# Optimization experiments

Hardware: AMD Instinct MI355X
Metric: run time of the kernel (lower is better)

Reference implementation:

```python
import jax, jax.numpy as jnp
import numpy as np

NUM_HEADS = 16
HEAD_DIM = 64
TOP_K_TILES = 8
TILE_SIZE = 16
ROPE_BASE = 10000.0


def make_freqs_cis(seq_len, head_dim):
    # [seq, head_dim//2] complex64, standard RoPE frequencies
    inv_freq = 1.0 / (ROPE_BASE ** (jnp.arange(0, head_dim, 2, dtype=jnp.float32) / head_dim))
    angles = jnp.arange(seq_len, dtype=jnp.float32)[:, None] * inv_freq[None, :]
    return jax.lax.complex(jnp.cos(angles), jnp.sin(angles))


def apply_rope(xq, xk, freqs_cis):
    # xq, xk: [b, h, s, d]; pairs adjacent channels as (real, imag)
    xq_ = xq.astype(jnp.float32).reshape(*xq.shape[:-1], -1, 2)
    xk_ = xk.astype(jnp.float32).reshape(*xk.shape[:-1], -1, 2)
    xq_c = jax.lax.complex(xq_[..., 0], xq_[..., 1])
    xk_c = jax.lax.complex(xk_[..., 0], xk_[..., 1])
    f = freqs_cis[None, None, :xq.shape[2], :]
    xq_r = xq_c * f
    xk_r = xk_c * f
    xq_out = jnp.stack([xq_r.real, xq_r.imag], axis=-1).reshape(xq.shape)
    xk_out = jnp.stack([xk_r.real, xk_r.imag], axis=-1).reshape(xk.shape)
    return xq_out.astype(xq.dtype), xk_out.astype(xk.dtype)


def setup_inputs() -> dict:
    key = jax.random.key(0)
    ks = jax.random.split(key, 5)
    B, S, D = 2, 2048, 1024
    scale = 1.0 / np.sqrt(D)
    return {
        "x": jax.random.normal(ks[0], (B, S, D), dtype=jnp.float32),
        "wq": jax.random.normal(ks[1], (D, NUM_HEADS * HEAD_DIM), dtype=jnp.float32) * scale,
        "wk": jax.random.normal(ks[2], (D, NUM_HEADS * HEAD_DIM), dtype=jnp.float32) * scale,
        "wv": jax.random.normal(ks[3], (D, NUM_HEADS * HEAD_DIM), dtype=jnp.float32) * scale,
        "wo": jax.random.normal(ks[4], (NUM_HEADS * HEAD_DIM, D), dtype=jnp.float32) * scale,
    }


def reference(x, wq, wk, wv, wo):
    batch, seq_len, _ = x.shape
    q = (x @ wq).reshape(batch, seq_len, NUM_HEADS, HEAD_DIM)
    k = (x @ wk).reshape(batch, seq_len, NUM_HEADS, HEAD_DIM)
    v = (x @ wv).reshape(batch, seq_len, NUM_HEADS, HEAD_DIM)

    freqs_cis = make_freqs_cis(seq_len, HEAD_DIM)
    q_t = jnp.transpose(q, (0, 2, 1, 3))
    k_t = jnp.transpose(k, (0, 2, 1, 3))
    q_t, k_t = apply_rope(q_t, k_t, freqs_cis)
    q = jnp.transpose(q_t, (0, 2, 1, 3))
    k = jnp.transpose(k_t, (0, 2, 1, 3))

    logits = jnp.einsum('bqhd,bkhd->bhqk', q, k) / jnp.sqrt(jnp.float32(HEAD_DIM))
    causal = jnp.tril(jnp.ones((seq_len, seq_len), dtype=bool))
    logits = jnp.where(causal[None, None, :, :], logits, -1e10)
    weights = jax.nn.softmax(logits, axis=-1)  # [b, h, q, k]

    # Scout: tile-max-pool last token's attention probs + top-k tile selection
    last_token_probs = weights[:, :, -1, :]  # [b, h, k]
    pad_len = (TILE_SIZE - seq_len % TILE_SIZE) % TILE_SIZE
    if pad_len > 0:
        last_token_probs = jnp.pad(last_token_probs, ((0, 0), (0, 0), (0, pad_len)))
    num_tiles = last_token_probs.shape[-1] // TILE_SIZE
    tile_scores = jnp.max(
        last_token_probs.reshape(batch, NUM_HEADS, num_tiles, TILE_SIZE), axis=-1)
    _, top_tile_indices = jax.lax.top_k(tile_scores, TOP_K_TILES)  # [b, h, top_k]

    output = jnp.einsum('bhqk,bkhd->bqhd', weights, v)
    output = output.reshape(batch, seq_len, NUM_HEADS * HEAD_DIM)
    output = output @ wo
    return output, top_tile_indices
```

## Files before the change

kernel.cpp:

```cpp
#include <hip/hip_runtime.h>

#define B_ 2
#define S_ 2048
#define E_ 1024
#define H_ 16
#define D_ 64
#define BS_ (B_*S_)
#define PSTR 76

typedef unsigned short u16;
typedef __attribute__((ext_vector_type(8))) short short8;
typedef __attribute__((ext_vector_type(4))) float floatx4;
typedef __bf16 bf16x8 __attribute__((ext_vector_type(8)));

__device__ __forceinline__ u16 f2bf(float f) {
    unsigned int u = __builtin_bit_cast(unsigned int, f);
    u += 0x7FFFu + ((u >> 16) & 1u);
    return (u16)(u >> 16);
}
__device__ __forceinline__ float bf2f(u16 h) {
    return __builtin_bit_cast(float, (unsigned int)h << 16);
}
__device__ __forceinline__ floatx4 mfma16(short8 a, short8 b, floatx4 c) {
    return __builtin_amdgcn_mfma_f32_16x16x32_bf16(
        __builtin_bit_cast(bf16x8, a), __builtin_bit_cast(bf16x8, b), c, 0, 0, 0);
}
__device__ __forceinline__ void gload_lds16(const void* g, void* l) {
    __builtin_amdgcn_global_load_lds(
        (const __attribute__((address_space(1))) unsigned int*)g,
        (__attribute__((address_space(3))) unsigned int*)l, 16, 0, 0);
}


__global__ __launch_bounds__(256) void rope_table_kernel(float* __restrict__ cost,
                                                         float* __restrict__ sint) {
    int idx = blockIdx.x * 256 + threadIdx.x;
    int s = idx >> 5, i = idx & 31;
    float inv = powf(10000.0f, -(float)i / 32.0f);
    float a = (float)s * inv;
    cost[idx] = cosf(a);
    sint[idx] = sinf(a);
}

__global__ __launch_bounds__(256) void convert_x_kernel(const float* __restrict__ X,
                                                        u16* __restrict__ xcat) {
    int i = blockIdx.x * 256 + threadIdx.x;
    int row = i >> 8, c4 = (i & 255) * 4;
    float4 v = ((const float4*)X)[i];
    u16 h0 = f2bf(v.x), h1 = f2bf(v.y), h2 = f2bf(v.z), h3 = f2bf(v.w);
    uint2 o;
    o.x = (unsigned)h0 | ((unsigned)h1 << 16);
    o.y = (unsigned)h2 | ((unsigned)h3 << 16);
    *(uint2*)&xcat[(size_t)row * 2048 + c4] = o;
    u16 l0 = f2bf(v.x - bf2f(h0)), l1 = f2bf(v.y - bf2f(h1));
    u16 l2 = f2bf(v.z - bf2f(h2)), l3 = f2bf(v.w - bf2f(h3));
    uint2 ol;
    ol.x = (unsigned)l0 | ((unsigned)l1 << 16);
    ol.y = (unsigned)l2 | ((unsigned)l3 << 16);
    *(uint2*)&xcat[(size_t)row * 2048 + 1024 + c4] = ol;
}

__global__ __launch_bounds__(256) void transpose_w4_kernel(const float* __restrict__ wq,
                                                           const float* __restrict__ wk,
                                                           const float* __restrict__ wv,
                                                           const float* __restrict__ wo,
                                                           u16* __restrict__ wqt,
                                                           u16* __restrict__ wkt,
                                                           u16* __restrict__ wkres,
                                                           u16* __restrict__ wvt,
                                                           u16* __restrict__ wot) {
    __shared__ float t[32][33];
    int bx = blockIdx.x;
    int which = bx >> 10, sub = bx & 1023;
    const float* W = which == 0 ? wq : which == 1 ? wk : which == 2 ? wv : wo;
    u16* Wt = which == 0 ? wqt : which == 1 ? wkt : which == 2 ? wvt : wot;
    int tk = (sub >> 5) * 32, tn = (sub & 31) * 32;
    int tx = threadIdx.x & 31, ty = threadIdx.x >> 5;
    for (int i = 0; i < 32; i += 8)
        t[ty + i][tx] = W[(size_t)(tk + ty + i) * E_ + tn + tx];
    __syncthreads();
    for (int i = 0; i < 32; i += 8) {
        float v = t[tx][ty + i];
        u16 hi = f2bf(v);
        Wt[(size_t)(tn + ty + i) * E_ + tk + tx] = hi;
        if (which == 1) {
            wkres[(size_t)(tn + ty + i) * 2048 + tk + tx] = f2bf(v - bf2f(hi));
            wkres[(size_t)(tn + ty + i) * 2048 + 1024 + tk + tx] = hi;
        }
    }
}


__device__ __forceinline__ void stage_swz(const u16* __restrict__ src, int row0, int k0,
                                          int stride, u16* lds, int tid) {
    int wv = tid >> 6, ln = tid & 63;
    int swz = (((ln & 7) ^ (ln >> 3)) << 3);
    int rr = ln >> 3;
#pragma unroll
    for (int i = 0; i < 4; ++i) {
        int seg = i * 4 + wv;
        gload_lds16(&src[(size_t)(row0 + seg * 8 + rr) * stride + k0 + swz],
                    (char*)lds + (size_t)seg * 1024);
    }
}

__device__ __forceinline__ void gemm_body(const u16* lA, const u16* lB,
                                          floatx4 (*acc)[4], int lane, int wave) {
    int wm = (wave >> 1) * 64, wn = (wave & 1) * 64;
    int lr = lane & 15, lq = lane >> 4, r7 = lr & 7;
#pragma unroll
    for (int half = 0; half < 2; ++half) {
        int xo = (((half * 4 + lq) ^ r7) << 3);
        short8 afr[4], bfr[4];
#pragma unroll
        for (int mi = 0; mi < 4; ++mi)
            afr[mi] = *(const short8*)&lA[(wm + mi * 16 + lr) * 64 + xo];
#pragma unroll
        for (int ni = 0; ni < 4; ++ni)
            bfr[ni] = *(const short8*)&lB[(wn + ni * 16 + lr) * 64 + xo];
        __builtin_amdgcn_s_setprio(1);
#pragma unroll
        for (int mi = 0; mi < 4; ++mi)
#pragma unroll
            for (int ni = 0; ni < 4; ++ni)
                acc[mi][ni] = mfma16(afr[mi], bfr[ni], acc[mi][ni]);
        __builtin_amdgcn_s_setprio(0);
    }
}

__device__ __forceinline__ void gemm_write(float* __restrict__ C, floatx4 (*acc)[4],
                                           int m0, int n0, int N, int lane, int wave) {
    int wm = (wave >> 1) * 64, wn = (wave & 1) * 64;
    int lr = lane & 15, lq = lane >> 4;
#pragma unroll
    for (int mi = 0; mi < 4; ++mi)
#pragma unroll
        for (int ni = 0; ni < 4; ++ni)
#pragma unroll
            for (int r = 0; r < 4; ++r)
                C[(size_t)(m0 + wm + mi * 16 + lq * 4 + r) * N + n0 + wn + ni * 16 + lr]
                    = acc[mi][ni][r];
}

__device__ __forceinline__ void rope_epilogue(floatx4 (*acc)[4], int m0, int n0,
                                              const float* __restrict__ cost,
                                              const float* __restrict__ sint,
                                              const float* __restrict__ qlast,
                                              u16* __restrict__ dstb,
                                              float* __restrict__ tscores,
                                              int lane, int wave) {
    int wm = (wave >> 1) * 64, wn = (wave & 1) * 64;
    int lr = lane & 15, lq = lane >> 4;
    int odd = lr & 1;
    int h = (n0 + wn) >> 6;
    int bq = m0 >> 11;
    int s0 = m0 & 2047;
    float qr[4];
    if (qlast) {
#pragma unroll
        for (int ni = 0; ni < 4; ++ni) {
            int d = ni * 16 + lr;
            int i = d >> 1;
            float qv = qlast[(size_t)bq * E_ + h * 64 + d];
            float qp = __shfl_xor(qv, 1);
            float c = cost[2047 * 32 + i], sn = sint[2047 * 32 + i];
            qr[ni] = odd ? (qp * sn + qv * c) : (qv * c - qp * sn);
        }
    }
    float dotp[4][4];
#pragma unroll
    for (int mi = 0; mi < 4; ++mi)
#pragma unroll
        for (int r = 0; r < 4; ++r) dotp[mi][r] = 0.f;
#pragma unroll
    for (int ni = 0; ni < 4; ++ni) {
        int d = ni * 16 + lr;
        int i = d >> 1;
#pragma unroll
        for (int mi = 0; mi < 4; ++mi) {
#pragma unroll
            for (int r = 0; r < 4; ++r) {
                int row = m0 + wm + mi * 16 + lq * 4 + r;
                int s = row & 2047;
                float own = acc[mi][ni][r];
                float par = __shfl_xor(own, 1);
                float c = cost[s * 32 + i], sn = sint[s * 32 + i];
                float out = odd ? (par * sn + own * c) : (own * c - par * sn);
                dstb[(((size_t)(bq * 16 + h)) * S_ + s) * 64 + d] = f2bf(out);
                if (qlast) dotp[mi][r] += out * qr[ni];
            }
        }
    }
    if (qlast) {
#pragma unroll
        for (int mi = 0; mi < 4; ++mi) {
            float tm = -1e30f;
#pragma unroll
            for (int r = 0; r < 4; ++r) {
                float dv = dotp[mi][r];
                dv += __shfl_xor(dv, 1);
                dv += __shfl_xor(dv, 2);
                dv += __shfl_xor(dv, 4);
                dv += __shfl_xor(dv, 8);
                tm = fmaxf(tm, dv);
            }
            tm = fmaxf(tm, __shfl_xor(tm, 16));
            tm = fmaxf(tm, __shfl_xor(tm, 32));
            if (lane == 0)
                tscores[(size_t)(bq * 16 + h) * 128 + (s0 >> 4) + (wm >> 4) + mi] = tm;
        }
    }
}

__device__ __forceinline__ void v_epilogue(floatx4 (*acc)[4], int m0, int n0,
                                           u16* vt, u16* __restrict__ vtb,
                                           int lane, int wave, int tid) {
    int wm = (wave >> 1) * 64, wn = (wave & 1) * 64;
    int lr = lane & 15, lq = lane >> 4;
#pragma unroll
    for (int ni = 0; ni < 4; ++ni) {
        int dcol = wn + ni * 16 + lr;
#pragma unroll
        for (int mi = 0; mi < 4; ++mi)
#pragma unroll
            for (int r = 0; r < 4; ++r)
                vt[dcol * 136 + wm + mi * 16 + lq * 4 + r] = f2bf(acc[mi][ni][r]);
    }
    __syncthreads();
    int dcol = tid >> 1, sh = (tid & 1) * 64;
    int colg = n0 + dcol, h = colg >> 6, d = colg & 63;
    int bq = m0 >> 11, s0 = m0 & 2047;
    size_t base = (((size_t)(bq * 16 + h)) * 64 + d) * S_ + s0 + sh;
#pragma unroll
    for (int c = 0; c < 8; ++c)
        *(uint4*)&vtb[base + c * 8] = *(const uint4*)&vt[dcol * 136 + sh + c * 8];
}

__global__ __launch_bounds__(256) void proj_gemm_kernel(const u16* __restrict__ xcat,
                                                        const u16* __restrict__ wqt,
                                                        const u16* __restrict__ wkt,
                                                        const u16* __restrict__ wkres,
                                                        const u16* __restrict__ wvt,
                                                        const float* __restrict__ cost,
                                                        const float* __restrict__ sint,
                                                        const float* __restrict__ qlast,
                                                        u16* __restrict__ qb,
                                                        u16* __restrict__ kb,
                                                        float* __restrict__ tscores,
                                                        u16* __restrict__ vtb) {
    __shared__ __align__(16) u16 lsbuf[17408];
    u16* lA = lsbuf;
    u16* lB = lsbuf + 8192;
    int bx = blockIdx.x;
    int role = bx >> 8;
    int idx = bx & 255;
    int xcd = idx & 7, loc = idx >> 3;
    int m0 = (xcd * 4 + (loc & 3)) * 128;
    int n0 = (loc >> 2) * 128;
    int tid = threadIdx.x, lane = tid & 63, wave = tid >> 6;

    floatx4 acc[4][4];
#pragma unroll
    for (int i = 0; i < 4; ++i)
#pragma unroll
        for (int j = 0; j < 4; ++j) acc[i][j] = (floatx4){0.f, 0.f, 0.f, 0.f};

    if (role == 0) {
        for (int k0 = 0; k0 < 1024; k0 += 64) {
            stage_swz(xcat, m0, k0, 2048, lA, tid);
            stage_swz(wkt, n0, k0, 1024, lB, tid);
            __syncthreads();
            gemm_body(lA, lB, acc, lane, wave);
            __syncthreads();
        }
        for (int k0 = 0; k0 < 2048; k0 += 64) {
            stage_swz(xcat, m0, k0, 2048, lA, tid);
            stage_swz(wkres, n0, k0, 2048, lB, tid);
            __syncthreads();
            gemm_body(lA, lB, acc, lane, wave);
            __syncthreads();
        }
        rope_epilogue(acc, m0, n0, cost, sint, qlast, kb, tscores, lane, wave);
    } else if (role == 1) {
        for (int k0 = 0; k0 < 1024; k0 += 64) {
            stage_swz(xcat, m0, k0, 2048, lA, tid);
            stage_swz(wqt, n0, k0, 1024, lB, tid);
            __syncthreads();
            gemm_body(lA, lB, acc, lane, wave);
            __syncthreads();
        }
        rope_epilogue(acc, m0, n0, cost, sint, (const float*)nullptr, qb,
                      (float*)nullptr, lane, wave);
    } else {
        for (int k0 = 0; k0 < 1024; k0 += 64) {
            stage_swz(xcat, m0, k0, 2048, lA, tid);
            stage_swz(wvt, n0, k0, 1024, lB, tid);
            __syncthreads();
            gemm_body(lA, lB, acc, lane, wave);
            __syncthreads();
        }
        v_epilogue(acc, m0, n0, lsbuf, vtb, lane, wave, tid);
    }
}

__global__ __launch_bounds__(256) void gemm_bf16_kernel(const u16* __restrict__ A,
                                                        const u16* __restrict__ Bt,
                                                        float* __restrict__ C,
                                                        int M, int N, int Kd) {
    __shared__ __align__(16) u16 lA[128 * 64];
    __shared__ __align__(16) u16 lB[128 * 64];
    int nwg = (M / 128) * (N / 128);
    int bx = blockIdx.x;
    int q = nwg >> 3, rr = nwg & 7, xcd = bx & 7, pos = bx >> 3;
    int lbx = (xcd < rr ? xcd * (q + 1) : rr * (q + 1) + (xcd - rr) * q) + pos;
    int nbn = N / 128;
    int m0 = (lbx / nbn) * 128, n0 = (lbx % nbn) * 128;
    int tid = threadIdx.x, lane = tid & 63, wave = tid >> 6;

    floatx4 acc[4][4];
#pragma unroll
    for (int i = 0; i < 4; ++i)
#pragma unroll
        for (int j = 0; j < 4; ++j) acc[i][j] = (floatx4){0.f, 0.f, 0.f, 0.f};

    for (int k0 = 0; k0 < Kd; k0 += 64) {
        stage_swz(A, m0, k0, Kd, lA, tid);
        stage_swz(Bt, n0, k0, Kd, lB, tid);
        __syncthreads();
        gemm_body(lA, lB, acc, lane, wave);
        __syncthreads();
    }
    gemm_write(C, acc, m0, n0, N, lane, wave);
}

__global__ __launch_bounds__(256) void qlast_kernel(const float* __restrict__ x,
                                                    const float* __restrict__ wq,
                                                    float* __restrict__ qlast) {
    __shared__ float red[8][32];
    int bx = blockIdx.x;
    int b = bx >> 5, c0 = (bx & 31) * 32;
    int cl = threadIdx.x & 31, kc = threadIdx.x >> 5;
    const float* xr = &x[((size_t)b * S_ + (S_ - 1)) * E_ + kc * 128];
    const float* wp = &wq[(size_t)(kc * 128) * E_ + c0 + cl];
    float acc = 0.f;
#pragma unroll 4
    for (int e = 0; e < 128; ++e) acc = fmaf(xr[e], wp[(size_t)e * E_], acc);
    red[kc][cl] = acc;
    __syncthreads();
    if (kc == 0) {
        float s = ((red[0][cl] + red[1][cl]) + (red[2][cl] + red[3][cl]))
                + ((red[4][cl] + red[5][cl]) + (red[6][cl] + red[7][cl]));
        qlast[(size_t)b * E_ + c0 + cl] = s;
    }
}

__device__ __forceinline__ void stage_kv(const u16* __restrict__ K, const u16* __restrict__ V,
                                         int n0, u16* kbuf, u16* vbuf, int wave, int lane) {
    int lr = lane & 15, lq = lane >> 4;
    if (wave < 2) {
#pragma unroll
        for (int i = 0; i < 4; ++i) {
            int sk = wave * 4 + i;
            int kt = sk >> 1, kh = (sk & 1) * 32;
            gload_lds16(&K[(size_t)(n0 + kt * 16 + lr) * D_ + kh + lq * 8],
                        kbuf + sk * 512);
        }
    } else {
#pragma unroll
        for (int i = 0; i < 4; ++i) {
            int sv = (wave - 2) * 4 + i;
            int c = sv >> 2, o = sv & 3;
            gload_lds16(&V[(size_t)(o * 16 + lr) * S_ + n0 + c * 32 + lq * 8],
                        vbuf + sv * 512);
        }
    }
}

__global__ __launch_bounds__(256) void flash_kernel(const u16* __restrict__ qb,
                                                    const u16* __restrict__ kb,
                                                    const u16* __restrict__ vtb,
                                                    u16* __restrict__ ab) {
    __shared__ __align__(16) u16 kls[2][8 * 512];
    __shared__ __align__(16) u16 vls[2][8 * 512];
    __shared__ __align__(16) u16 ldsP[4][16 * PSTR];
    int tid = threadIdx.x;
    int lane = tid & 63, wave = tid >> 6;
    int bx = blockIdx.x;
    int xcd = bx & 7, ii = bx >> 3;
    int hid = xcd + 8 * (ii & 3);
    int qc = 31 - (ii >> 2);
    int qt0 = qc * 64 + wave * 16;
    const u16* Q = qb + (size_t)hid * S_ * D_;
    const u16* K = kb + (size_t)hid * S_ * D_;
    const u16* V = vtb + (size_t)hid * D_ * S_;
    u16* lp = &ldsP[wave][0];
    int lr = lane & 15, lq = lane >> 4, lk = lq * 8;

    short8 qfr0 = *(const short8*)&Q[(size_t)(qt0 + lr) * D_ + lk];
    short8 qfr1 = *(const short8*)&Q[(size_t)(qt0 + lr) * D_ + 32 + lk];

    floatx4 o0 = {0,0,0,0}, o1 = {0,0,0,0}, o2 = {0,0,0,0}, o3 = {0,0,0,0};
    float m = -1e30f, l = 0.f;

    stage_kv(K, V, 0, kls[0], vls[0], wave, lane);
    asm volatile("s_waitcnt vmcnt(0)" ::: "memory");
    __syncthreads();

    for (int it = 0; it <= qc; ++it) {
        int n0 = it * 64;
        int buf = it & 1;
        const u16* kbuf = kls[buf];
        const u16* vbuf = vls[buf];
        if (it < qc)
            stage_kv(K, V, n0 + 64, kls[buf ^ 1], vls[buf ^ 1], wave, lane);

        short8 ka0[4], ka1[4];
#pragma unroll
        for (int kt = 0; kt < 4; ++kt) {
            ka0[kt] = *(const short8*)&kbuf[(kt * 2 + 0) * 512 + lane * 8];
            ka1[kt] = *(const short8*)&kbuf[(kt * 2 + 1) * 512 + lane * 8];
        }
        floatx4 st[4];
#pragma unroll
        for (int kt = 0; kt < 4; ++kt) st[kt] = (floatx4){0.f, 0.f, 0.f, 0.f};
        __builtin_amdgcn_s_setprio(1);
#pragma unroll
        for (int kt = 0; kt < 4; ++kt) {
            st[kt] = mfma16(ka0[kt], qfr0, st[kt]);
            st[kt] = mfma16(ka1[kt], qfr1, st[kt]);
        }
        __builtin_amdgcn_s_setprio(0);

        const float SC = 0.18033688011112042f;
        int rem = qt0 + 16 - n0;
        float sv[4][4];
        float bmax = -1e30f;
        if (rem >= 80) {
#pragma unroll
            for (int kt = 0; kt < 4; ++kt)
#pragma unroll
                for (int r = 0; r < 4; ++r) {
                    float s = st[kt][r] * SC;
                    sv[kt][r] = s;
                    bmax = fmaxf(bmax, s);
                }
        } else {
#pragma unroll
            for (int kt = 0; kt < 4; ++kt)
#pragma unroll
                for (int r = 0; r < 4; ++r) {
                    int k = n0 + kt * 16 + lq * 4 + r;
                    float s = (k <= qt0 + lr) ? st[kt][r] * SC : -1e30f;
                    sv[kt][r] = s;
                    bmax = fmaxf(bmax, s);
                }
        }
        bmax = fmaxf(bmax, __shfl_xor(bmax, 16));
        bmax = fmaxf(bmax, __shfl_xor(bmax, 32));
        if (!__all(bmax <= m + 8.0f)) {
            float mn = fmaxf(m, bmax);
            float alpha = __builtin_amdgcn_exp2f(m - mn);
            m = mn;
            l *= alpha;
            float af[4];
#pragma unroll
            for (int r = 0; r < 4; ++r) af[r] = __shfl(alpha, lq * 4 + r);
#pragma unroll
            for (int r = 0; r < 4; ++r) {
                o0[r] *= af[r]; o1[r] *= af[r]; o2[r] *= af[r]; o3[r] *= af[r];
            }
        }
        float ps = 0.f;
#pragma unroll
        for (int kt = 0; kt < 4; ++kt) {
            float p0 = __builtin_amdgcn_exp2f(sv[kt][0] - m);
            float p1 = __builtin_amdgcn_exp2f(sv[kt][1] - m);
            float p2 = __builtin_amdgcn_exp2f(sv[kt][2] - m);
            float p3 = __builtin_amdgcn_exp2f(sv[kt][3] - m);
            ps += (p0 + p1) + (p2 + p3);
            unsigned wlo, whi;
            asm("v_cvt_pk_bf16_f32 %0, %1, %2" : "=v"(wlo) : "v"(p0), "v"(p1));
            asm("v_cvt_pk_bf16_f32 %0, %1, %2" : "=v"(whi) : "v"(p2), "v"(p3));
            *(uint2*)&lp[lr * PSTR + kt * 16 + lq * 4] = (uint2){wlo, whi};
        }
        ps += __shfl_xor(ps, 16);
        ps += __shfl_xor(ps, 32);
        l += ps;

        short8 vv[2][4];
#pragma unroll
        for (int c = 0; c < 2; ++c)
#pragma unroll
            for (int o = 0; o < 4; ++o)
                vv[c][o] = *(const short8*)&vbuf[(c * 4 + o) * 512 + lane * 8];
        asm volatile("s_waitcnt lgkmcnt(0)" ::: "memory");
        __builtin_amdgcn_s_setprio(1);
#pragma unroll
        for (int c = 0; c < 2; ++c) {
            uint2 plo = *(const uint2*)&lp[lr * PSTR + c * 32 + lk];
            uint2 phi = *(const uint2*)&lp[lr * PSTR + c * 32 + lk + 4];
            short8 pfr = __builtin_bit_cast(short8, (uint4){plo.x, plo.y, phi.x, phi.y});
            o0 = mfma16(pfr, vv[c][0], o0);
            o1 = mfma16(pfr, vv[c][1], o1);
            o2 = mfma16(pfr, vv[c][2], o2);
            o3 = mfma16(pfr, vv[c][3], o3);
        }
        __builtin_amdgcn_s_setprio(0);

        if (it < qc) {
            asm volatile("s_waitcnt vmcnt(0)" ::: "memory");
            __syncthreads();
        }
    }
    float li[4];
#pragma unroll
    for (int r = 0; r < 4; ++r) li[r] = 1.0f / __shfl(l, lq * 4 + r);
    int b = hid >> 4, h = hid & 15;
    size_t orow_base = ((size_t)b * S_ + qt0 + lq * 4) * E_ + h * D_;
#pragma unroll
    for (int r = 0; r < 4; ++r) {
        size_t rb = orow_base + (size_t)r * E_;
        ab[rb + 0  + lr] = f2bf(o0[r] * li[r]);
        ab[rb + 16 + lr] = f2bf(o1[r] * li[r]);
        ab[rb + 32 + lr] = f2bf(o2[r] * li[r]);
        ab[rb + 48 + lr] = f2bf(o3[r] * li[r]);
    }
}

__global__ __launch_bounds__(64) void topk_select_kernel(const float* __restrict__ tscores,
                                                         float* __restrict__ oidx) {
    int bh = blockIdx.x, tid = threadIdx.x;
    float v0 = tscores[bh * 128 + tid], v1 = tscores[bh * 128 + 64 + tid];
    float va, vb; int ia, ib;
    if (v1 > v0) { va = v1; ia = tid + 64; vb = v0; ib = tid; }
    else         { va = v0; ia = tid;      vb = v1; ib = tid + 64; }
    float cv = va; int ci = ia; int used = 0;
    for (int t = 0; t < 8; ++t) {
        float bv = cv; int bi = ci;
#pragma unroll
        for (int mk = 1; mk < 64; mk <<= 1) {
            float ov = __shfl_xor(bv, mk);
            int oi = __shfl_xor(bi, mk);
            if (ov > bv || (ov == bv && oi < bi)) { bv = ov; bi = oi; }
        }
        if (tid == 0) oidx[bh * 8 + t] = (float)bi;
        if (ci == bi) {
            if (used == 0) { cv = vb; ci = ib; used = 1; }
            else           { cv = -3e30f; ci = 1 << 20; }
        }
    }
}

extern "C" void kernel_launch(void* const* d_in, const int* in_sizes, int n_in,
                              void* d_out, int out_size, void* d_ws, size_t ws_size,
                              hipStream_t stream) {
    (void)in_sizes; (void)n_in; (void)out_size; (void)ws_size;
    const float* x  = (const float*)d_in[0];
    const float* wq = (const float*)d_in[1];
    const float* wk = (const float*)d_in[2];
    const float* wv = (const float*)d_in[3];
    const float* wo = (const float*)d_in[4];
    float* out = (float*)d_out;

    char* wsp = (char*)d_ws;
    size_t off = 0;
    auto nxt = [&](size_t bytes) {
        char* p = wsp + off;
        off = (off + bytes + 255) & ~(size_t)255;
        return p;
    };
    u16* xcat  = (u16*)nxt((size_t)BS_ * 2048 * 2);
    u16* wqt   = (u16*)nxt((size_t)E_ * E_ * 2);
    u16* wkt   = (u16*)nxt((size_t)E_ * E_ * 2);
    u16* wkres = (u16*)nxt((size_t)E_ * 2048 * 2);
    u16* wvt   = (u16*)nxt((size_t)E_ * E_ * 2);
    u16* wot   = (u16*)nxt((size_t)E_ * E_ * 2);
    float* cost = (float*)nxt((size_t)S_ * 32 * 4);
    float* sint = (float*)nxt((size_t)S_ * 32 * 4);
    u16* qb    = (u16*)nxt((size_t)B_ * H_ * S_ * D_ * 2);
    u16* kb    = (u16*)nxt((size_t)B_ * H_ * S_ * D_ * 2);
    u16* vtb   = (u16*)nxt((size_t)B_ * H_ * S_ * D_ * 2);
    u16* ab    = (u16*)nxt((size_t)BS_ * E_ * 2);
    float* qlast = (float*)nxt((size_t)B_ * E_ * 4);
    float* tscores = (float*)nxt((size_t)B_ * H_ * 128 * 4);

    hipLaunchKernelGGL(rope_table_kernel, dim3(S_ * 32 / 256), dim3(256), 0, stream, cost, sint);
    hipLaunchKernelGGL(convert_x_kernel, dim3(BS_ * E_ / 4 / 256), dim3(256), 0, stream, x, xcat);
    hipLaunchKernelGGL(transpose_w4_kernel, dim3(4096), dim3(256), 0, stream,
                       wq, wk, wv, wo, wqt, wkt, wkres, wvt, wot);
    hipLaunchKernelGGL(qlast_kernel, dim3(64), dim3(256), 0, stream, x, wq, qlast);

    hipLaunchKernelGGL(proj_gemm_kernel, dim3(768), dim3(256), 0, stream,
                       xcat, wqt, wkt, wkres, wvt, cost, sint, qlast,
                       qb, kb, tscores, vtb);

    hipLaunchKernelGGL(flash_kernel, dim3(B_ * H_ * (S_ / 64)), dim3(256), 0, stream,
                       qb, kb, vtb, ab);

    hipLaunchKernelGGL(topk_select_kernel, dim3(B_ * H_), dim3(64), 0, stream,
                       tscores, out + (size_t)BS_ * E_);

    hipLaunchKernelGGL(gemm_bf16_kernel, dim3(256), dim3(256), 0, stream, ab, wot, out,
                       BS_, E_, E_);
}
```

Baseline: 223.2 us.

## Fuse prep kernels and double-buffer LDS in projection and output GEMMs

Merges the four preprocessing kernels (x split-convert, weight transposes, RoPE table, last-token q) into one launch to cut launch gaps. Adds double-buffered LDS staging in the Q/V projection and the output GEMM, so the next k-tile's global-to-LDS loads overlap the current MFMA work. For the K projection, the three split-precision products (hi*hi, hi*res, res*hi) now share one staging pass per k-step instead of two separate loops. LDS use per block rises to 64KB, which may lower occupancy.

Result: no change. 221.8 us (-0.6%).

```diff
diff --git a/kernel.cpp b/kernel.cpp
--- a/kernel.cpp
+++ b/kernel.cpp
@@ -31,61 +31,80 @@
         (__attribute__((address_space(3))) unsigned int*)l, 16, 0, 0);
 }
 
-
-__global__ __launch_bounds__(256) void rope_table_kernel(float* __restrict__ cost,
-                                                         float* __restrict__ sint) {
-    int idx = blockIdx.x * 256 + threadIdx.x;
-    int s = idx >> 5, i = idx & 31;
-    float inv = powf(10000.0f, -(float)i / 32.0f);
-    float a = (float)s * inv;
-    cost[idx] = cosf(a);
-    sint[idx] = sinf(a);
-}
-
-__global__ __launch_bounds__(256) void convert_x_kernel(const float* __restrict__ X,
-                                                        u16* __restrict__ xcat) {
-    int i = blockIdx.x * 256 + threadIdx.x;
-    int row = i >> 8, c4 = (i & 255) * 4;
-    float4 v = ((const float4*)X)[i];
-    u16 h0 = f2bf(v.x), h1 = f2bf(v.y), h2 = f2bf(v.z), h3 = f2bf(v.w);
-    uint2 o;
-    o.x = (unsigned)h0 | ((unsigned)h1 << 16);
-    o.y = (unsigned)h2 | ((unsigned)h3 << 16);
-    *(uint2*)&xcat[(size_t)row * 2048 + c4] = o;
-    u16 l0 = f2bf(v.x - bf2f(h0)), l1 = f2bf(v.y - bf2f(h1));
-    u16 l2 = f2bf(v.z - bf2f(h2)), l3 = f2bf(v.w - bf2f(h3));
-    uint2 ol;
-    ol.x = (unsigned)l0 | ((unsigned)l1 << 16);
-    ol.y = (unsigned)l2 | ((unsigned)l3 << 16);
-    *(uint2*)&xcat[(size_t)row * 2048 + 1024 + c4] = ol;
-}
-
-__global__ __launch_bounds__(256) void transpose_w4_kernel(const float* __restrict__ wq,
-                                                           const float* __restrict__ wk,
-                                                           const float* __restrict__ wv,
-                                                           const float* __restrict__ wo,
-                                                           u16* __restrict__ wqt,
-                                                           u16* __restrict__ wkt,
-                                                           u16* __restrict__ wkres,
-                                                           u16* __restrict__ wvt,
-                                                           u16* __restrict__ wot) {
+__global__ __launch_bounds__(256) void prep_kernel(const float* __restrict__ x,
+                                                   const float* __restrict__ wq,
+                                                   const float* __restrict__ wk,
+                                                   const float* __restrict__ wv,
+                                                   const float* __restrict__ wo,
+                                                   u16* __restrict__ xcat,
+                                                   u16* __restrict__ wqt,
+                                                   u16* __restrict__ wkt,
+                                                   u16* __restrict__ wkres,
+                                                   u16* __restrict__ wvt,
+                                                   u16* __restrict__ wot,
+                                                   float* __restrict__ cost,
+                                                   float* __restrict__ sint,
+                                                   float* __restrict__ qlast) {
     __shared__ float t[32][33];
     int bx = blockIdx.x;
-    int which = bx >> 10, sub = bx & 1023;
-    const float* W = which == 0 ? wq : which == 1 ? wk : which == 2 ? wv : wo;
-    u16* Wt = which == 0 ? wqt : which == 1 ? wkt : which == 2 ? wvt : wot;
-    int tk = (sub >> 5) * 32, tn = (sub & 31) * 32;
-    int tx = threadIdx.x & 31, ty = threadIdx.x >> 5;
-    for (int i = 0; i < 32; i += 8)
-        t[ty + i][tx] = W[(size_t)(tk + ty + i) * E_ + tn + tx];
-    __syncthreads();
-    for (int i = 0; i < 32; i += 8) {
-        float v = t[tx][ty + i];
-        u16 hi = f2bf(v);
-        Wt[(size_t)(tn + ty + i) * E_ + tk + tx] = hi;
-        if (which == 1) {
-            wkres[(size_t)(tn + ty + i) * 2048 + tk + tx] = f2bf(v - bf2f(hi));
-            wkres[(size_t)(tn + ty + i) * 2048 + 1024 + tk + tx] = hi;
+    int tid = threadIdx.x;
+    if (bx < 4096) {
+        int i = bx * 256 + tid;
+        int row = i >> 8, c4 = (i & 255) * 4;
+        float4 v = ((const float4*)x)[i];
+        u16 h0 = f2bf(v.x), h1 = f2bf(v.y), h2 = f2bf(v.z), h3 = f2bf(v.w);
+        uint2 o;
+        o.x = (unsigned)h0 | ((unsigned)h1 << 16);
+        o.y = (unsigned)h2 | ((unsigned)h3 << 16);
+        *(uint2*)&xcat[(size_t)row * 2048 + c4] = o;
+        u16 l0 = f2bf(v.x - bf2f(h0)), l1 = f2bf(v.y - bf2f(h1));
+        u16 l2 = f2bf(v.z - bf2f(h2)), l3 = f2bf(v.w - bf2f(h3));
+        uint2 ol;
+        ol.x = (unsigned)l0 | ((unsigned)l1 << 16);
+        ol.y = (unsigned)l2 | ((unsigned)l3 << 16);
+        *(uint2*)&xcat[(size_t)row * 2048 + 1024 + c4] = ol;
+    } else if (bx < 8192) {
+        int sub = bx - 4096;
+        int which = sub >> 10, s2 = sub & 1023;
+        const float* W = which == 0 ? wq : which == 1 ? wk : which == 2 ? wv : wo;
+        u16* Wt = which == 0 ? wqt : which == 1 ? wkt : which == 2 ? wvt : wot;
+        int tk = (s2 >> 5) * 32, tn = (s2 & 31) * 32;
+        int tx = tid & 31, ty = tid >> 5;
+        for (int i = 0; i < 32; i += 8)
+            t[ty + i][tx] = W[(size_t)(tk + ty + i) * E_ + tn + tx];
+        __syncthreads();
+        for (int i = 0; i < 32; i += 8) {
+            float v = t[tx][ty + i];
+            u16 hi = f2bf(v);
+            Wt[(size_t)(tn + ty + i) * E_ + tk + tx] = hi;
+            if (which == 1) {
+                wkres[(size_t)(tn + ty + i) * 2048 + tk + tx] = f2bf(v - bf2f(hi));
+                wkres[(size_t)(tn + ty + i) * 2048 + 1024 + tk + tx] = hi;
+            }
+        }
+    } else if (bx < 8448) {
+        int idx = (bx - 8192) * 256 + tid;
+        int s = idx >> 5, i = idx & 31;
+        float inv = powf(10000.0f, -(float)i / 32.0f);
+        float a = (float)s * inv;
+        cost[idx] = cosf(a);
+        sint[idx] = sinf(a);
+    } else {
+        float* red = &t[0][0];
+        int b2 = bx - 8448;
+        int b = b2 >> 5, c0 = (b2 & 31) * 32;
+        int cl = tid & 31, kc = tid >> 5;
+        const float* xr = &x[((size_t)b * S_ + (S_ - 1)) * E_ + kc * 128];
+        const float* wp = &wq[(size_t)(kc * 128) * E_ + c0 + cl];
+        float acc = 0.f;
+#pragma unroll 4
+        for (int e = 0; e < 128; ++e) acc = fmaf(xr[e], wp[(size_t)e * E_], acc);
+        red[kc * 32 + cl] = acc;
+        __syncthreads();
+        if (kc == 0) {
+            float s = ((red[0 * 32 + cl] + red[1 * 32 + cl]) + (red[2 * 32 + cl] + red[3 * 32 + cl]))
+                    + ((red[4 * 32 + cl] + red[5 * 32 + cl]) + (red[6 * 32 + cl] + red[7 * 32 + cl]));
+            qlast[(size_t)b * E_ + c0 + cl] = s;
         }
     }
 }
@@ -248,9 +267,11 @@
                                                         u16* __restrict__ kb,
                                                         float* __restrict__ tscores,
                                                         u16* __restrict__ vtb) {
-    __shared__ __align__(16) u16 lsbuf[17408];
-    u16* lA = lsbuf;
-    u16* lB = lsbuf + 8192;
+    __shared__ __align__(16) u16 lds4[4 * 8192];
+    u16* T0 = lds4;
+    u16* T1 = lds4 + 8192;
+    u16* T2 = lds4 + 16384;
+    u16* T3 = lds4 + 24576;
     int bx = blockIdx.x;
     int role = bx >> 8;
     int idx = bx & 255;
@@ -267,39 +288,41 @@
 
     if (role == 0) {
         for (int k0 = 0; k0 < 1024; k0 += 64) {
-            stage_swz(xcat, m0, k0, 2048, lA, tid);
-            stage_swz(wkt, n0, k0, 1024, lB, tid);
+            stage_swz(xcat, m0, k0, 2048, T0, tid);
+            stage_swz(xcat, m0, k0 + 1024, 2048, T1, tid);
+            stage_swz(wkt, n0, k0, 1024, T2, tid);
+            stage_swz(wkres, n0, k0, 2048, T3, tid);
+            asm volatile("s_waitcnt vmcnt(0)" ::: "memory");
             __syncthreads();
-            gemm_body(lA, lB, acc, lane, wave);
+            gemm_body(T0, T2, acc, lane, wave);
+            gemm_body(T0, T3, acc, lane, wave);
+            gemm_body(T1, T2, acc, lane, wave);
             __syncthreads();
         }
-        for (int k0 = 0; k0 < 2048; k0 += 64) {
-            stage_swz(xcat, m0, k0, 2048, lA, tid);
-            stage_swz(wkres, n0, k0, 2048, lB, tid);
+        rope_epilogue(acc, m0, n0, cost, sint, qlast, kb, tscores, lane, wave);
+    } else {
+        const u16* Bt = (role == 1) ? wqt : wvt;
+        stage_swz(xcat, m0, 0, 2048, T0, tid);
+        stage_swz(Bt, n0, 0, 1024, T2, tid);
+        asm volatile("s_waitcnt vmcnt(0)" ::: "memory");
+        __syncthreads();
+        for (int step = 0; step < 16; ++step) {
+            int buf = step & 1;
+            u16* Ac = buf ? T1 : T0;
+            u16* Bc = buf ? T3 : T2;
+            if (step < 15) {
+                stage_swz(xcat, m0, (step + 1) * 64, 2048, buf ? T0 : T1, tid);
+                stage_swz(Bt, n0, (step + 1) * 64, 1024, buf ? T2 : T3, tid);
+            }
+            gemm_body(Ac, Bc, acc, lane, wave);
+            asm volatile("s_waitcnt vmcnt(0)" ::: "memory");
             __syncthreads();
-            gemm_body(lA, lB, acc, lane, wave);
-            __syncthreads();
-        }
-        rope_epilogue(acc, m0, n0, cost, sint, qlast, kb, tscores, lane, wave);
-    } else if (role == 1) {
-        for (int k0 = 0; k0 < 1024; k0 += 64) {
-            stage_swz(xcat, m0, k0, 2048, lA, tid);
-            stage_swz(wqt, n0, k0, 1024, lB, tid);
-            __syncthreads();
-            gemm_body(lA, lB, acc, lane, wave);
-            __syncthreads();
-        }
-        rope_epilogue(acc, m0, n0, cost, sint, (const float*)nullptr, qb,
-                      (float*)nullptr, lane, wave);
-    } else {
-        for (int k0 = 0; k0 < 1024; k0 += 64) {
-            stage_swz(xcat, m0, k0, 2048, lA, tid);
-            stage_swz(wvt, n0, k0, 1024, lB, tid);
-            __syncthreads();
-            gemm_body(lA, lB, acc, lane, wave);
-            __syncthreads();
-        }
-        v_epilogue(acc, m0, n0, lsbuf, vtb, lane, wave, tid);
+        }
+        if (role == 1)
+            rope_epilogue(acc, m0, n0, cost, sint, (const float*)nullptr, qb,
+                          (float*)nullptr, lane, wave);
+        else
+            v_epilogue(acc, m0, n0, lds4, vtb, lane, wave, tid);
     }
 }
 
@@ -307,8 +330,11 @@
                                                         const u16* __restrict__ Bt,
                                                         float* __restrict__ C,
                                                         int M, int N, int Kd) {
-    __shared__ __align__(16) u16 lA[128 * 64];
-    __shared__ __align__(16) u16 lB[128 * 64];
+    __shared__ __align__(16) u16 lds4[4 * 8192];
+    u16* T0 = lds4;
+    u16* T1 = lds4 + 8192;
+    u16* T2 = lds4 + 16384;
+    u16* T3 = lds4 + 24576;
     int nwg = (M / 128) * (N / 128);
     int bx = blockIdx.x;
     int q = nwg >> 3, rr = nwg & 7, xcd = bx & 7, pos = bx >> 3;
@@ -323,35 +349,24 @@
 #pragma unroll
         for (int j = 0; j < 4; ++j) acc[i][j] = (floatx4){0.f, 0.f, 0.f, 0.f};
 
-    for (int k0 = 0; k0 < Kd; k0 += 64) {
-        stage_swz(A, m0, k0, Kd, lA, tid);
-        stage_swz(Bt, n0, k0, Kd, lB, tid);
+    int nsteps = Kd / 64;
+    stage_swz(A, m0, 0, Kd, T0, tid);
+    stage_swz(Bt, n0, 0, Kd, T2, tid);
+    asm volatile("s_waitcnt vmcnt(0)" ::: "memory");
+    __syncthreads();
+    for (int step = 0; step < nsteps; ++step) {
+        int buf = step & 1;
+        u16* Ac = buf ? T1 : T0;
+        u16* Bc = buf ? T3 : T2;
+        if (step + 1 < nsteps) {
+            stage_swz(A, m0, (step + 1) * 64, Kd, buf ? T0 : T1, tid);
+            stage_swz(Bt, n0, (step + 1) * 64, Kd, buf ? T2 : T3, tid);
+        }
+        gemm_body(Ac, Bc, acc, lane, wave);
+        asm volatile("s_waitcnt vmcnt(0)" ::: "memory");
         __syncthreads();
-        gemm_body(lA, lB, acc, lane, wave);
-        __syncthreads();
     }
     gemm_write(C, acc, m0, n0, N, lane, wave);
-}
-
-__global__ __launch_bounds__(256) void qlast_kernel(const float* __restrict__ x,
-                                                    const float* __restrict__ wq,
-                                                    float* __restrict__ qlast) {
-    __shared__ float red[8][32];
-    int bx = blockIdx.x;
-    int b = bx >> 5, c0 = (bx & 31) * 32;
-    int cl = threadIdx.x & 31, kc = threadIdx.x >> 5;
-    const float* xr = &x[((size_t)b * S_ + (S_ - 1)) * E_ + kc * 128];
-    const float* wp = &wq[(size_t)(kc * 128) * E_ + c0 + cl];
-    float acc = 0.f;
-#pragma unroll 4
-    for (int e = 0; e < 128; ++e) acc = fmaf(xr[e], wp[(size_t)e * E_], acc);
-    red[kc][cl] = acc;
-    __syncthreads();
-    if (kc == 0) {
-        float s = ((red[0][cl] + red[1][cl]) + (red[2][cl] + red[3][cl]))
-                + ((red[4][cl] + red[5][cl]) + (red[6][cl] + red[7][cl]));
-        qlast[(size_t)b * E_ + c0 + cl] = s;
-    }
 }
 
 __device__ __forceinline__ void stage_kv(const u16* __restrict__ K, const u16* __restrict__ V,
@@ -584,11 +599,9 @@
     float* qlast = (float*)nxt((size_t)B_ * E_ * 4);
     float* tscores = (float*)nxt((size_t)B_ * H_ * 128 * 4);
 
-    hipLaunchKernelGGL(rope_table_kernel, dim3(S_ * 32 / 256), dim3(256), 0, stream, cost, sint);
-    hipLaunchKernelGGL(convert_x_kernel, dim3(BS_ * E_ / 4 / 256), dim3(256), 0, stream, x, xcat);
-    hipLaunchKernelGGL(transpose_w4_kernel, dim3(4096), dim3(256), 0, stream,
-                       wq, wk, wv, wo, wqt, wkt, wkres, wvt, wot);
-    hipLaunchKernelGGL(qlast_kernel, dim3(64), dim3(256), 0, stream, x, wq, qlast);
+    hipLaunchKernelGGL(prep_kernel, dim3(8512), dim3(256), 0, stream,
+                       x, wq, wk, wv, wo, xcat, wqt, wkt, wkres, wvt, wot,
+                       cost, sint, qlast);
 
     hipLaunchKernelGGL(proj_gemm_kernel, dim3(768), dim3(256), 0, stream,
                        xcat, wqt, wkt, wkres, wvt, cost, sint, qlast,
```
